# Kernel tuning notes

Hardware: AMD Instinct MI355X
Metric: run time of the kernel (lower is better)

The kernel has to match this reference:

```python
import jax
jax.config.update('jax_enable_x64', True)  # exact int64 phase products (torch builds phasors in complex128)
import jax.numpy as jnp
import numpy as np

L = 393216          # seq_length, divisible by Locc=4, K=12, mmse_block=12
K = 12              # ktc=4 -> K=12
LOCC = 4            # _compute_locc for ktc=4
U, P = 8, 4         # max_users, max_ports_per_user
BLK = 12            # mmse_block_size
SEARCH_MIN, SEARCH_MAX = -10, 10


def setup_inputs() -> dict:
    key = jax.random.key(0)
    k1, k2, k3 = jax.random.split(key, 3)
    ls_real = jax.random.normal(k1, (L,), dtype=jnp.float32)
    ls_imag = jax.random.normal(k2, (L,), dtype=jnp.float32)
    cyclic_shifts = jax.random.randint(k3, (U, P), 0, K)  # int, values in [0, K)
    return {"ls_real": ls_real, "ls_imag": ls_imag, "cyclic_shifts": cyclic_shifts}


def _phasor(m):
    """exp(1j*2*pi*m*n/L) for each m in the [UP] vector -> [UP, L] complex64.
    Phase reduced mod L in exact int64 before float conversion for accuracy."""
    n = jnp.arange(L, dtype=jnp.int64)
    r = (m.astype(jnp.int64)[:, None] * n[None, :]) % L      # exact
    ang = (2.0 * np.pi / L) * r.astype(jnp.float32)
    return jnp.exp(1j * ang).astype(jnp.complex64)


def _forward(ls, cyclic_shifts):
    shifts = cyclic_shifts.reshape(-1)                        # [UP]
    ideal_peak = ((K - shifts) % K) * L // K                  # [UP]

    # --- timing offset search in +/-10 window around ideal peak (CIR domain) ---
    h_time = jnp.fft.ifft(ls)                                 # IDFT
    h_mag = jnp.abs(h_time) ** 2                              # [L]
    offs = jnp.arange(SEARCH_MIN, SEARCH_MAX + 1)             # [21]
    win = (ideal_peak[:, None] + offs[None, :]) % L           # [UP, 21]
    T = offs[jnp.argmax(h_mag[win], axis=1)]                  # [UP] timing offsets
    m = T + ideal_peak                                        # [UP]

    ph_m = _phasor(m)                                         # [UP, L]
    ph_T = _phasor(T)                                         # [UP, L]

    # --- per-port cyclic de-shift, OCC demux (avg of 4), linear interp back to L ---
    h_up = ls[None, :] * ph_m                                 # [UP, L]
    h_avg = h_up.reshape(-1, L // LOCC, LOCC).mean(-1)        # [UP, L/4]
    orig_idx = (LOCC - 1) / 2.0 + LOCC * jnp.arange(L // LOCC, dtype=jnp.float32)
    new_idx = jnp.arange(L, dtype=jnp.float32)
    interp1 = jax.vmap(lambda y: jnp.interp(new_idx, orig_idx, y))
    h_interp = (interp1(h_avg.real.astype(jnp.float32))
                + 1j * interp1(h_avg.imag.astype(jnp.float32))).astype(jnp.complex64)  # [UP, L]

    # --- residual reconstruction and re-addition per port ---
    h_recon = jnp.sum(h_interp * jnp.conj(ph_m), axis=0)      # [L]
    residual = ls - h_recon
    h_wr = h_interp + residual[None, :] * ph_m                # [UP, L]

    # --- noise power estimate from adjacent-sample differences ---
    diff = ls[1:] - ls[:-1]
    noise_power = jnp.mean(jnp.abs(diff) ** 2) / 2

    # --- block MMSE: h_mmse = C (C + R)^-1 h with default C = I, R = sigma^2 I ---
    C = jnp.eye(BLK, dtype=jnp.complex64)
    Rm = noise_power.astype(jnp.complex64) * jnp.eye(BLK, dtype=jnp.complex64)
    M = C @ jnp.linalg.inv(C + Rm)                            # [12, 12]
    hb = h_wr.reshape(-1, L // BLK, BLK)                      # [UP, L/12, 12]
    h_mmse = jnp.einsum('ij,ubj->ubi', M, hb).reshape(-1, L)  # [UP, L]

    # --- align back by conj timing phasor ---
    return h_mmse * jnp.conj(ph_T)                            # [UP, L] complex64


def reference(ls_real, ls_imag, cyclic_shifts):
    ls = (ls_real + 1j * ls_imag).astype(jnp.complex64)
    return _forward(ls, cyclic_shifts)
```

## Files before the change

kernel.cpp:

```cpp
#include <hip/hip_runtime.h>
#include <math.h>

#define L_TOT 393216
#define L_D4  98304
#define NPORT 32
#define NPEAK 12
#define NOFF  21
#define NCAND 252
#define TILE  1536
#define NBLK  (L_TOT / TILE)
#define HALF_ELEMS 12582912ull

__device__ float2 g_F[NBLK * NCAND];
__device__ double g_npart[NBLK];
__device__ int    g_prm[96];
__device__ float  g_scale[1];

__constant__ double c_cos12[12] = {1.0, 0.8660254037844387, 0.5, 0.0, -0.5,
  -0.8660254037844387, -1.0, -0.8660254037844387, -0.5, 0.0, 0.5, 0.8660254037844387};
__constant__ double c_sin12[12] = {0.0, 0.5, 0.8660254037844387, 1.0,
  0.8660254037844387, 0.5, 0.0, -0.5, -0.8660254037844387, -1.0,
  -0.8660254037844387, -0.5};

__device__ __forceinline__ void interp_coords(int n, int* j0, float* f) {
  float x = ((float)n - 1.5f) * 0.25f;
  if (x <= 0.f)                    { *j0 = 0;        *f = 0.f; }
  else if (x >= (float)(L_D4 - 1)) { *j0 = L_D4 - 2; *f = 1.f; }
  else { int jj = (int)x; *j0 = jj; *f = x - (float)jj; }
}

__device__ __forceinline__ float2 zpowS(float2 z, float2 z2, float2 z4, float2 z8, int T) {
  int t = T < 0 ? -T : T;
  float cr = 1.f, ci = 0.f;
  if (t & 1) { cr = z.x; ci = z.y; }
  if (t & 2) { float a = cr*z2.x - ci*z2.y, b = cr*z2.y + ci*z2.x; cr = a; ci = b; }
  if (t & 4) { float a = cr*z4.x - ci*z4.y, b = cr*z4.y + ci*z4.x; cr = a; ci = b; }
  if (t & 8) { float a = cr*z8.x - ci*z8.y, b = cr*z8.y + ci*z8.x; cr = a; ci = b; }
  if (T < 0) ci = -ci;
  return make_float2(cr, ci);
}

__global__ __launch_bounds__(256) void search_kernel(
    const float* __restrict__ lsr, const float* __restrict__ lsi) {
  __shared__ float2 sh_ls[TILE + 1];
  __shared__ float2 sh_z[TILE];
  __shared__ float2 sh_red[NCAND * NOFF];
  const float w = (float)(2.0 * M_PI / (double)L_TOT);
  int tid = threadIdx.x;
  int KB = blockIdx.x * TILE;
  for (int i = tid; i < TILE + 1; i += 256) {
    int k = KB + i; if (k > L_TOT - 1) k = L_TOT - 1;
    sh_ls[i] = make_float2(lsr[k], lsi[k]);
  }
  for (int i = tid; i < TILE; i += 256) {
    float s, c; __sincosf(w * (float)(KB + i), &s, &c);
    sh_z[i] = make_float2(c, s);
  }
  __syncthreads();

  if (tid < NCAND) {
    int r = tid % 12, lane = tid / 12;
    float accr[NOFF], acci[NOFF];
#pragma unroll
    for (int d = 0; d < NOFF; ++d) { accr[d] = 0.f; acci[d] = 0.f; }
    for (int q = lane; q < TILE / 12; q += 21) {
      int kl = 12 * q + r;
      float2 y = sh_ls[kl];
      float2 z = sh_z[kl];
      accr[10] += y.x; acci[10] += y.y;
      float cpr = y.x, cpi = y.y, cmr = y.x, cmi = y.y;
#pragma unroll
      for (int d = 1; d <= 10; ++d) {
        float tr = cpr*z.x - cpi*z.y, ti = cpr*z.y + cpi*z.x; cpr = tr; cpi = ti;
        accr[10 + d] += cpr; acci[10 + d] += cpi;
        tr = cmr*z.x + cmi*z.y; ti = cmi*z.x - cmr*z.y; cmr = tr; cmi = ti;
        accr[10 - d] += cmr; acci[10 - d] += cmi;
      }
    }
#pragma unroll
    for (int d = 0; d < NOFF; ++d)
      sh_red[tid * NOFF + d] = make_float2(accr[d], acci[d]);
  }
  double nacc = 0.0;
  int top = (KB + TILE <= L_TOT - 1) ? TILE : (L_TOT - 1 - KB);
  for (int i = tid; i < top; i += 256) {
    float2 a = sh_ls[i], b = sh_ls[i + 1];
    float dr = b.x - a.x, di = b.y - a.y;
    nacc += (double)(dr * dr + di * di);
  }
  __syncthreads();
  if (tid < NCAND) {
    int r = tid / NOFF, dd = tid - r * NOFF;
    float fr = 0.f, fi = 0.f;
    for (int lane = 0; lane < 21; ++lane) {
      float2 v = sh_red[(lane * 12 + r) * NOFF + dd];
      fr += v.x; fi += v.y;
    }
    g_F[blockIdx.x * NCAND + tid] = make_float2(fr, fi);
  }
  __syncthreads();
  double* nb = (double*)sh_red;
  nb[tid] = nacc;
  __syncthreads();
  for (int t = 128; t > 0; t >>= 1) {
    if (tid < t) nb[tid] += nb[tid + t];
    __syncthreads();
  }
  if (tid == 0) g_npart[blockIdx.x] = nb[0];
}

__global__ __launch_bounds__(256) void select_kernel(
    const int* __restrict__ shifts) {
  __shared__ double sGr[NCAND], sGi[NCAND];
  __shared__ double hmag[NCAND];
  __shared__ double nred[256];
  int tid = threadIdx.x;
  if (tid < NCAND) {
    double gr = 0.0, gi = 0.0;
    for (int b = 0; b < NBLK; ++b) {
      float2 v = g_F[b * NCAND + tid];
      gr += (double)v.x; gi += (double)v.y;
    }
    sGr[tid] = gr; sGi[tid] = gi;
  }
  nred[tid] = g_npart[tid];
  __syncthreads();
  if (tid < NCAND) {
    int p = tid / NOFF, dd = tid - p * NOFF;
    double sr = 0.0, si = 0.0;
    for (int r = 0; r < 12; ++r) {
      int idx = (p * r) % 12;
      double gr = sGr[r * NOFF + dd], gi = sGi[r * NOFF + dd];
      sr += c_cos12[idx] * gr - c_sin12[idx] * gi;
      si += c_cos12[idx] * gi + c_sin12[idx] * gr;
    }
    hmag[tid] = sr * sr + si * si;
  }
  __syncthreads();
  for (int t = 128; t > 0; t >>= 1) {
    if (tid < t) nred[tid] += nred[tid + t];
    __syncthreads();
  }
  if (tid < NPORT) {
    int s = shifts[tid];
    int p = (NPEAK - (s % NPEAK)) % NPEAK;
    double best = -1.0; int bd = 0;
    for (int d = 0; d < NOFF; ++d) {
      double v = hmag[p * NOFF + d];
      if (v > best) { best = v; bd = d; }
    }
    int T = bd - 10;
    int m = T + p * (L_TOT / NPEAK);
    if (m < 0) m += L_TOT;
    g_prm[tid]      = T;
    g_prm[32 + tid] = p;
    g_prm[64 + tid] = m;
  }
  if (tid == 0) {
    double npow = nred[0] / (double)(L_TOT - 1) * 0.5;
    g_scale[0] = (float)(1.0 / (1.0 + npow));
  }
}

__global__ __launch_bounds__(256) void fused_kernel(
    const float* __restrict__ lsr, const float* __restrict__ lsi,
    float* __restrict__ out, unsigned long long out_elems) {
  __shared__ float2 sh_ls[264];
  __shared__ float2 sh_h[NPORT][67];
  __shared__ float2 sh_tbl[144];
  __shared__ float2 sh_stp[NPORT];
  __shared__ int    sm_T[NPORT], sm_p[NPORT], sm_m[NPORT];
  __shared__ float  sm_scale;

  const float w = (float)(2.0 * M_PI / (double)L_TOT);
  int tid = threadIdx.x;
  int N0 = blockIdx.x * 256;
  int JBASE; float fd;
  interp_coords(N0, &JBASE, &fd);
  int K0 = 4 * JBASE;

  if (tid < NPORT) {
    sm_T[tid] = g_prm[tid]; sm_p[tid] = g_prm[32 + tid];
    int m = g_prm[64 + tid]; sm_m[tid] = m;
    float s, c; __sincosf(w * (float)m, &s, &c);
    sh_stp[tid] = make_float2(c, s);
  }
  if (tid == 0) sm_scale = g_scale[0];
  if (tid < 144) {
    int p = tid / 12, r = tid - p * 12;
    int idx = (p * r) % 12;
    float s, c; __sincosf((float)(2.0 * M_PI / 12.0) * (float)idx, &s, &c);
    sh_tbl[tid] = make_float2(c, s);
  }
  for (int i = tid; i < 264; i += 256) {
    int k = K0 + i; if (k > L_TOT - 1) k = L_TOT - 1;
    sh_ls[i] = make_float2(lsr[k], lsi[k]);
  }
  __syncthreads();

  for (int e = tid; e < NPORT * 66; e += 256) {
    int u = e & 31, jj = e >> 5;
    int j = JBASE + jj; if (j > L_D4 - 1) j = L_D4 - 1;
    int k0 = 4 * j, kk = k0 - K0;
    unsigned rr = (unsigned)(((long long)sm_m[u] * k0) % L_TOT);
    float phs, phc; __sincosf(w * (float)rr, &phs, &phc);
    float2 stp = sh_stp[u];
    float sr = 0.f, si = 0.f;
#pragma unroll
    for (int t = 0; t < 4; ++t) {
      float2 v = sh_ls[kk + t];
      sr += v.x * phc - v.y * phs;
      si += v.x * phs + v.y * phc;
      float a = phc * stp.x - phs * stp.y, b = phc * stp.y + phs * stp.x;
      phc = a; phs = b;
    }
    sh_h[u][jj] = make_float2(0.25f * sr, 0.25f * si);
  }
  __syncthreads();

  int n = N0 + tid;
  int j0; float f;
  interp_coords(n, &j0, &f);
  int jj0 = j0 - JBASE;
  int r12 = n % 12;
  float2 lsn = sh_ls[n - K0];
  float zs, zc; __sincosf(w * (float)n, &zs, &zc);
  float2 zn = make_float2(zc, zs);
  float2 z2 = make_float2(zn.x*zn.x - zn.y*zn.y, 2.f*zn.x*zn.y);
  float2 z4 = make_float2(z2.x*z2.x - z2.y*z2.y, 2.f*z2.x*z2.y);
  float2 z8 = make_float2(z4.x*z4.x - z4.y*z4.y, 2.f*z4.x*z4.y);

  float aAr[NPORT], aAi[NPORT];
  float rcr = 0.f, rci = 0.f;
#pragma unroll
  for (int u = 0; u < NPORT; ++u) {
    int T = __builtin_amdgcn_readfirstlane(sm_T[u]);
    int p = __builtin_amdgcn_readfirstlane(sm_p[u]);
    float2 zT = zpowS(zn, z2, z4, z8, T);
    float2 tb = sh_tbl[p * 12 + r12];
    float2 y0 = sh_h[u][jj0], y1 = sh_h[u][jj0 + 1];
    float hr = y0.x + f * (y1.x - y0.x);
    float hi = y0.y + f * (y1.y - y0.y);
    float Ar = hr * zT.x + hi * zT.y;
    float Ai = hi * zT.x - hr * zT.y;
    aAr[u] = Ar; aAi[u] = Ai;
    rcr += Ar * tb.x + Ai * tb.y;
    rci += Ai * tb.x - Ar * tb.y;
  }
  float resr = lsn.x - rcr, resi = lsn.y - rci;
  float scl = sm_scale;

  if (out_elems >= 2ull * HALF_ELEMS) {
#pragma unroll
    for (int u = 0; u < NPORT; ++u) {
      int p = __builtin_amdgcn_readfirstlane(sm_p[u]);
      float2 tb = sh_tbl[p * 12 + r12];
      float orr = aAr[u] + resr * tb.x - resi * tb.y;
      float oii = aAi[u] + resr * tb.y + resi * tb.x;
      unsigned long long o = (unsigned long long)u * L_TOT + (unsigned)n;
      out[o] = scl * orr;
      out[HALF_ELEMS + o] = scl * oii;
    }
  } else {
#pragma unroll
    for (int u = 0; u < NPORT; ++u) {
      int p = __builtin_amdgcn_readfirstlane(sm_p[u]);
      float2 tb = sh_tbl[p * 12 + r12];
      float orr = aAr[u] + resr * tb.x - resi * tb.y;
      float oii = aAi[u] + resr * tb.y + resi * tb.x;
      unsigned long long o = (unsigned long long)u * L_TOT + (unsigned)n;
      if (o < out_elems)              out[o] = scl * orr;
      if (HALF_ELEMS + o < out_elems) out[HALF_ELEMS + o] = scl * oii;
    }
  }
}

extern "C" void kernel_launch(void* const* d_in, const int* in_sizes, int n_in,
                              void* d_out, int out_size, void* d_ws, size_t ws_size,
                              hipStream_t stream) {
  const float* lsr    = (const float*)d_in[0];
  const float* lsi    = (const float*)d_in[1];
  const int*   shifts = (const int*)d_in[2];
  float* out = (float*)d_out;

  if (in_sizes[0] != L_TOT || in_sizes[1] != L_TOT) return;

  unsigned long long out_elems = (unsigned long long)(out_size > 0 ? out_size : 0);

  search_kernel<<<NBLK, 256, 0, stream>>>(lsr, lsi);
  select_kernel<<<1, 256, 0, stream>>>(shifts);
  fused_kernel<<<L_TOT / 256, 256, 0, stream>>>(lsr, lsi, out, out_elems);
}
```

Measured before the change: 121.7 us.

## Deduplicate ports sharing the same peak into slots and compute each once

Ports with the same cyclic shift share the same peak and timing offset, so their per-port outputs are identical. The select kernel now groups the 32 ports into at most 12 distinct slots, recording a count and port bitmask for each. The fused kernel runs the demux, interpolation and reconstruction once per slot, weights the reconstruction by the count, and writes the result to every port in the mask. This cuts arithmetic and shared-memory work, but the output writes are unchanged and now go through a data-dependent mask loop, so a store-bound kernel may gain little.

After: 122.0 us. No clear change (+0.2%).

```diff
diff --git a/kernel.cpp b/kernel.cpp
--- a/kernel.cpp
+++ b/kernel.cpp
@@ -9,6 +9,7 @@
 #define NCAND 252
 #define TILE  1536
 #define NBLK  (L_TOT / TILE)
+#define NSLOT 12
 #define HALF_ELEMS 12582912ull
 
 __device__ float2 g_F[NBLK * NCAND];
@@ -114,6 +115,7 @@
   __shared__ double sGr[NCAND], sGi[NCAND];
   __shared__ double hmag[NCAND];
   __shared__ double nred[256];
+  __shared__ int    sh_pu[NPORT], sh_Tu[NPORT];
   int tid = threadIdx.x;
   if (tid < NCAND) {
     double gr = 0.0, gi = 0.0;
@@ -149,14 +151,38 @@
       double v = hmag[p * NOFF + d];
       if (v > best) { best = v; bd = d; }
     }
-    int T = bd - 10;
-    int m = T + p * (L_TOT / NPEAK);
-    if (m < 0) m += L_TOT;
-    g_prm[tid]      = T;
-    g_prm[32 + tid] = p;
-    g_prm[64 + tid] = m;
-  }
+    sh_pu[tid] = p;
+    sh_Tu[tid] = bd - 10;
+  }
+  __syncthreads();
   if (tid == 0) {
+    int nd = 0;
+    int pv[NSLOT], tv[NSLOT], mv[NSLOT], cv[NSLOT]; unsigned msk[NSLOT];
+#pragma unroll
+    for (int s = 0; s < NSLOT; ++s) { pv[s] = 0; tv[s] = 0; mv[s] = 0; cv[s] = 0; msk[s] = 0u; }
+    for (int u = 0; u < NPORT; ++u) {
+      int p = sh_pu[u];
+      int slot = -1;
+      for (int s = 0; s < nd; ++s) if (pv[s] == p) { slot = s; break; }
+      if (slot < 0) {
+        slot = nd++;
+        pv[slot] = p; tv[slot] = sh_Tu[u];
+        int m = sh_Tu[u] + p * (L_TOT / NPEAK);
+        if (m < 0) m += L_TOT;
+        mv[slot] = m;
+      }
+      cv[slot] += 1;
+      msk[slot] |= (1u << u);
+    }
+    g_prm[0] = nd;
+#pragma unroll
+    for (int s = 0; s < NSLOT; ++s) {
+      g_prm[1 + s]  = pv[s];
+      g_prm[13 + s] = tv[s];
+      g_prm[25 + s] = mv[s];
+      g_prm[37 + s] = cv[s];
+      g_prm[49 + s] = (int)msk[s];
+    }
     double npow = nred[0] / (double)(L_TOT - 1) * 0.5;
     g_scale[0] = (float)(1.0 / (1.0 + npow));
   }
@@ -166,10 +192,11 @@
     const float* __restrict__ lsr, const float* __restrict__ lsi,
     float* __restrict__ out, unsigned long long out_elems) {
   __shared__ float2 sh_ls[264];
-  __shared__ float2 sh_h[NPORT][67];
+  __shared__ float2 sh_h[16][67];
   __shared__ float2 sh_tbl[144];
-  __shared__ float2 sh_stp[NPORT];
-  __shared__ int    sm_T[NPORT], sm_p[NPORT], sm_m[NPORT];
+  __shared__ float2 sh_stp1[NSLOT];
+  __shared__ int    sm_T[NSLOT], sm_p[NSLOT], sm_m[NSLOT], sm_cnt[NSLOT], sm_msk[NSLOT];
+  __shared__ int    sm_nd;
   __shared__ float  sm_scale;
 
   const float w = (float)(2.0 * M_PI / (double)L_TOT);
@@ -179,13 +206,16 @@
   interp_coords(N0, &JBASE, &fd);
   int K0 = 4 * JBASE;
 
-  if (tid < NPORT) {
-    sm_T[tid] = g_prm[tid]; sm_p[tid] = g_prm[32 + tid];
-    int m = g_prm[64 + tid]; sm_m[tid] = m;
+  if (tid < NSLOT) {
+    sm_T[tid] = g_prm[13 + tid];
+    sm_p[tid] = g_prm[1 + tid];
+    int m = g_prm[25 + tid]; sm_m[tid] = m;
+    sm_cnt[tid] = g_prm[37 + tid];
+    sm_msk[tid] = g_prm[49 + tid];
     float s, c; __sincosf(w * (float)m, &s, &c);
-    sh_stp[tid] = make_float2(c, s);
-  }
-  if (tid == 0) sm_scale = g_scale[0];
+    sh_stp1[tid] = make_float2(c, s);
+  }
+  if (tid == 0) { sm_nd = g_prm[0]; sm_scale = g_scale[0]; }
   if (tid < 144) {
     int p = tid / 12, r = tid - p * 12;
     int idx = (p * r) % 12;
@@ -198,23 +228,27 @@
   }
   __syncthreads();
 
-  for (int e = tid; e < NPORT * 66; e += 256) {
-    int u = e & 31, jj = e >> 5;
-    int j = JBASE + jj; if (j > L_D4 - 1) j = L_D4 - 1;
-    int k0 = 4 * j, kk = k0 - K0;
-    unsigned rr = (unsigned)(((long long)sm_m[u] * k0) % L_TOT);
-    float phs, phc; __sincosf(w * (float)rr, &phs, &phc);
-    float2 stp = sh_stp[u];
-    float sr = 0.f, si = 0.f;
-#pragma unroll
-    for (int t = 0; t < 4; ++t) {
-      float2 v = sh_ls[kk + t];
-      sr += v.x * phc - v.y * phs;
-      si += v.x * phs + v.y * phc;
-      float a = phc * stp.x - phs * stp.y, b = phc * stp.y + phs * stp.x;
-      phc = a; phs = b;
-    }
-    sh_h[u][jj] = make_float2(0.25f * sr, 0.25f * si);
+  int nd = __builtin_amdgcn_readfirstlane(sm_nd);
+
+  for (int e = tid; e < 66 * 16; e += 256) {
+    int s = e & 15, jj = e >> 4;
+    if (s < nd) {
+      int j = JBASE + jj; if (j > L_D4 - 1) j = L_D4 - 1;
+      int k0 = 4 * j, kk = k0 - K0;
+      unsigned rr = (unsigned)(((long long)sm_m[s] * k0) % L_TOT);
+      float phs, phc; __sincosf(w * (float)rr, &phs, &phc);
+      float2 stp = sh_stp1[s];
+      float sr = 0.f, si = 0.f;
+#pragma unroll
+      for (int t = 0; t < 4; ++t) {
+        float2 v = sh_ls[kk + t];
+        sr += v.x * phc - v.y * phs;
+        si += v.x * phs + v.y * phc;
+        float a = phc * stp.x - phs * stp.y, b = phc * stp.y + phs * stp.x;
+        phc = a; phs = b;
+      }
+      sh_h[s][jj] = make_float2(0.25f * sr, 0.25f * si);
+    }
   }
   __syncthreads();
 
@@ -230,47 +264,49 @@
   float2 z4 = make_float2(z2.x*z2.x - z2.y*z2.y, 2.f*z2.x*z2.y);
   float2 z8 = make_float2(z4.x*z4.x - z4.y*z4.y, 2.f*z4.x*z4.y);
 
-  float aAr[NPORT], aAi[NPORT];
+  float aAr[NSLOT], aAi[NSLOT];
   float rcr = 0.f, rci = 0.f;
 #pragma unroll
-  for (int u = 0; u < NPORT; ++u) {
-    int T = __builtin_amdgcn_readfirstlane(sm_T[u]);
-    int p = __builtin_amdgcn_readfirstlane(sm_p[u]);
-    float2 zT = zpowS(zn, z2, z4, z8, T);
-    float2 tb = sh_tbl[p * 12 + r12];
-    float2 y0 = sh_h[u][jj0], y1 = sh_h[u][jj0 + 1];
-    float hr = y0.x + f * (y1.x - y0.x);
-    float hi = y0.y + f * (y1.y - y0.y);
-    float Ar = hr * zT.x + hi * zT.y;
-    float Ai = hi * zT.x - hr * zT.y;
-    aAr[u] = Ar; aAi[u] = Ai;
-    rcr += Ar * tb.x + Ai * tb.y;
-    rci += Ai * tb.x - Ar * tb.y;
+  for (int s = 0; s < NSLOT; ++s) {
+    if (s < nd) {
+      int T = __builtin_amdgcn_readfirstlane(sm_T[s]);
+      int p = __builtin_amdgcn_readfirstlane(sm_p[s]);
+      float cnt = (float)__builtin_amdgcn_readfirstlane(sm_cnt[s]);
+      float2 zT = zpowS(zn, z2, z4, z8, T);
+      float2 tb = sh_tbl[p * 12 + r12];
+      float2 y0 = sh_h[s][jj0], y1 = sh_h[s][jj0 + 1];
+      float hr = y0.x + f * (y1.x - y0.x);
+      float hi = y0.y + f * (y1.y - y0.y);
+      float Ar = hr * zT.x + hi * zT.y;
+      float Ai = hi * zT.x - hr * zT.y;
+      aAr[s] = Ar; aAi[s] = Ai;
+      rcr += cnt * (Ar * tb.x + Ai * tb.y);
+      rci += cnt * (Ai * tb.x - Ar * tb.y);
+    } else { aAr[s] = 0.f; aAi[s] = 0.f; }
   }
   float resr = lsn.x - rcr, resi = lsn.y - rci;
   float scl = sm_scale;
 
-  if (out_elems >= 2ull * HALF_ELEMS) {
-#pragma unroll
-    for (int u = 0; u < NPORT; ++u) {
-      int p = __builtin_amdgcn_readfirstlane(sm_p[u]);
+  bool full = (out_elems >= 2ull * HALF_ELEMS);
+#pragma unroll
+  for (int s = 0; s < NSLOT; ++s) {
+    if (s < nd) {
+      int p = __builtin_amdgcn_readfirstlane(sm_p[s]);
+      unsigned mask = (unsigned)__builtin_amdgcn_readfirstlane(sm_msk[s]);
       float2 tb = sh_tbl[p * 12 + r12];
-      float orr = aAr[u] + resr * tb.x - resi * tb.y;
-      float oii = aAi[u] + resr * tb.y + resi * tb.x;
-      unsigned long long o = (unsigned long long)u * L_TOT + (unsigned)n;
-      out[o] = scl * orr;
-      out[HALF_ELEMS + o] = scl * oii;
-    }
-  } else {
-#pragma unroll
-    for (int u = 0; u < NPORT; ++u) {
-      int p = __builtin_amdgcn_readfirstlane(sm_p[u]);
-      float2 tb = sh_tbl[p * 12 + r12];
-      float orr = aAr[u] + resr * tb.x - resi * tb.y;
-      float oii = aAi[u] + resr * tb.y + resi * tb.x;
-      unsigned long long o = (unsigned long long)u * L_TOT + (unsigned)n;
-      if (o < out_elems)              out[o] = scl * orr;
-      if (HALF_ELEMS + o < out_elems) out[HALF_ELEMS + o] = scl * oii;
+      float orr = scl * (aAr[s] + resr * tb.x - resi * tb.y);
+      float oii = scl * (aAi[s] + resr * tb.y + resi * tb.x);
+      while (mask) {
+        int u = __builtin_ctz(mask); mask &= mask - 1;
+        unsigned long long o = (unsigned long long)u * L_TOT + (unsigned)n;
+        if (full) {
+          out[o] = orr;
+          out[HALF_ELEMS + o] = oii;
+        } else {
+          if (o < out_elems)              out[o] = orr;
+          if (HALF_ELEMS + o < out_elems) out[HALF_ELEMS + o] = oii;
+        }
+      }
     }
   }
 }
```
